# Performance work log

Measured on AMD Instinct MI355X. Metric: run time of the kernel, lower is better.

Reference implementation:

```python
import jax, jax.numpy as jnp
import numpy as np

N_NODES = 50000
N_EDGES = 800000
IN_CH = 128
OUT_CH = 64
HEADS = 4
NEG_SLOPE = 0.2  # PyG GATConv default


def setup_inputs() -> dict:
    key = jax.random.key(0)
    k1, k2, k3, k4, k5 = jax.random.split(key, 5)
    x = jax.random.normal(k1, (N_NODES, IN_CH), dtype=jnp.float32)
    edge_index = jax.random.randint(k2, (2, N_EDGES), 0, N_NODES, dtype=jnp.int64)
    W = jax.random.normal(k3, (HEADS * OUT_CH, IN_CH), dtype=jnp.float32) * (1.0 / np.sqrt(IN_CH))
    att_src = jax.random.normal(k4, (HEADS, OUT_CH), dtype=jnp.float32) * (1.0 / np.sqrt(OUT_CH))
    att_dst = jax.random.normal(k5, (HEADS, OUT_CH), dtype=jnp.float32) * (1.0 / np.sqrt(OUT_CH))
    bias = jnp.zeros((OUT_CH,), dtype=jnp.float32)
    return {"x": x, "edge_index": edge_index, "W": W,
            "att_src": att_src, "att_dst": att_dst, "bias": bias}


def reference(x, edge_index, W, att_src, att_dst, bias):
    # GAT2NO_NORM.forward in eval mode: dropout == identity.
    N = x.shape[0]
    H, C = att_src.shape
    # PyG GATConv adds self-loops by default.
    loop = jnp.arange(N, dtype=edge_index.dtype)
    src = jnp.concatenate([edge_index[0], loop])  # message source j
    dst = jnp.concatenate([edge_index[1], loop])  # message target i
    # Linear projection, reshape to heads: [N, H, C]
    h = (x @ W.T).reshape(N, H, C)
    # Per-node attention halves: [N, H]
    a_src = jnp.einsum('nhc,hc->nh', h, att_src)
    a_dst = jnp.einsum('nhc,hc->nh', h, att_dst)
    # Per-edge raw score, LeakyReLU: [E, H]
    e = jax.nn.leaky_relu(a_src[src] + a_dst[dst], NEG_SLOPE)
    # Segment (edge-)softmax over incoming edges of each dst node.
    m = jax.lax.stop_gradient(jax.ops.segment_max(e, dst, num_segments=N))
    ex = jnp.exp(e - m[dst])
    denom = jax.ops.segment_sum(ex, dst, num_segments=N)
    alpha = ex / denom[dst]  # self-loops guarantee denom > 0
    # Weighted scatter-sum of messages: [N, H, C]
    msg = h[src] * alpha[:, :, None]
    out = jax.ops.segment_sum(msg, dst, num_segments=N)
    # concat=False -> mean over heads, then bias, then ReLU (module wrapper)
    out = out.mean(axis=1) + bias
    return jax.nn.relu(out)
```

## Files before the change

### kernel.cpp

```cpp
#include <hip/hip_runtime.h>
#include <hip/hip_fp16.h>
#include <math.h>

#define N_NODES 50000
#define N_EDGES 800000
#define IN_CH 128
#define PROJ_CH 256
#define OUT_CH 64
#define HEADS 4
#define NEG_SLOPE 0.2f
#define CAP 80
#define PROJ_BLOCKS 782
#define GRID_BLOCKS 3125

typedef _Float16 f16x8 __attribute__((ext_vector_type(8)));
typedef _Float16 f16x4 __attribute__((ext_vector_type(4)));
typedef float    f32x4 __attribute__((ext_vector_type(4)));

__device__ __forceinline__ float leaky(float v) {
    return v > 0.f ? v : NEG_SLOPE * v;
}

__global__ __launch_bounds__(256) void prep_kernel(
    const float* __restrict__ W, _Float16* __restrict__ Wfrag, int* __restrict__ cnt)
{
    int t = blockIdx.x * 256 + threadIdx.x;
    if (t < N_NODES) cnt[t] = 0;
    if (t < 4096) {
        int lane = t & 63;
        int n0i  = (t >> 6) & 3;
        int w    = (t >> 8) & 3;
        int k0i  = t >> 10;
        int oc = w * 64 + n0i * 16 + (lane & 15);
        int kb = k0i * 32 + (lane >> 4) * 8;
        const float* src = W + (size_t)oc * IN_CH + kb;
        f16x8 v;
#pragma unroll
        for (int j = 0; j < 8; ++j) v[j] = (_Float16)src[j];
        *(f16x8*)(Wfrag + (size_t)t * 8) = v;
    }
}

__global__ __launch_bounds__(256) void mega_kernel(
    const float* __restrict__ x, const _Float16* __restrict__ Wfrag,
    const float* __restrict__ att_src, const float* __restrict__ att_dst,
    const int* __restrict__ ei, int* __restrict__ cnt, unsigned short* __restrict__ csr,
    _Float16* __restrict__ h, float* __restrict__ a_src, float* __restrict__ a_dst)
{
    __shared__ _Float16 xs[64 * 136];
    const int tid = threadIdx.x;
    const int bid = blockIdx.x;

    const int e = bid * 256 + tid;
    const int esrc = ei[e];
    const int edst = ei[N_EDGES + e];

    if (bid >= PROJ_BLOCKS) {
        int pos = atomicAdd(&cnt[edst], 1);
        if (pos < CAP) csr[edst * CAP + pos] = (unsigned short)esrc;
        return;
    }

    const int w    = tid >> 6;
    const int lane = tid & 63;
    const int q    = lane >> 4;
    const int l15  = lane & 15;
    const int nb   = bid * 64;

    f16x8 B[4][4];
#pragma unroll
    for (int k0i = 0; k0i < 4; ++k0i)
#pragma unroll
        for (int n0i = 0; n0i < 4; ++n0i)
            B[k0i][n0i] = *(const f16x8*)(Wfrag +
                (size_t)(((k0i * 4 + w) * 4 + n0i) * 64 + lane) * 8);

#pragma unroll
    for (int r = 0; r < 8; ++r) {
        int v   = r * 256 + tid;
        int row = v >> 5;
        int c4  = v & 31;
        int grow = nb + row;
        if (grow > N_NODES - 1) grow = N_NODES - 1;
        float4 xv = *(const float4*)(x + (size_t)grow * IN_CH + c4 * 4);
        f16x4 hv;
        hv[0] = (_Float16)xv.x; hv[1] = (_Float16)xv.y;
        hv[2] = (_Float16)xv.z; hv[3] = (_Float16)xv.w;
        *(f16x4*)&xs[row * 136 + c4 * 4] = hv;
    }
    __syncthreads();

    const int pos = atomicAdd(&cnt[edst], 1);

    f32x4 acc[4][4];
#pragma unroll
    for (int m0i = 0; m0i < 4; ++m0i)
#pragma unroll
        for (int n0i = 0; n0i < 4; ++n0i)
            acc[m0i][n0i] = (f32x4){0.f, 0.f, 0.f, 0.f};

#pragma unroll
    for (int k0i = 0; k0i < 4; ++k0i) {
        f16x8 A[4];
#pragma unroll
        for (int m0i = 0; m0i < 4; ++m0i)
            A[m0i] = *(const f16x8*)&xs[(m0i * 16 + l15) * 136 + k0i * 32 + q * 8];
#pragma unroll
        for (int n0i = 0; n0i < 4; ++n0i)
#pragma unroll
            for (int m0i = 0; m0i < 4; ++m0i)
                acc[m0i][n0i] = __builtin_amdgcn_mfma_f32_16x16x32_f16(
                    A[m0i], B[k0i][n0i], acc[m0i][n0i], 0, 0, 0);
    }

    float att_s[4], att_d[4];
#pragma unroll
    for (int n0i = 0; n0i < 4; ++n0i) {
        att_s[n0i] = att_src[w * 64 + n0i * 16 + l15];
        att_d[n0i] = att_dst[w * 64 + n0i * 16 + l15];
    }

#pragma unroll
    for (int m0i = 0; m0i < 4; ++m0i) {
        float vs[4], vd[4];
#pragma unroll
        for (int r = 0; r < 4; ++r) {
            float s = 0.f, d = 0.f;
#pragma unroll
            for (int n0i = 0; n0i < 4; ++n0i) {
                s = fmaf(acc[m0i][n0i][r], att_s[n0i], s);
                d = fmaf(acc[m0i][n0i][r], att_d[n0i], d);
            }
            vs[r] = s; vd[r] = d;
        }
#pragma unroll
        for (int off = 1; off < 16; off <<= 1) {
#pragma unroll
            for (int r = 0; r < 4; ++r) {
                vs[r] += __shfl_xor(vs[r], off, 64);
                vd[r] += __shfl_xor(vd[r], off, 64);
            }
        }
#pragma unroll
        for (int r = 0; r < 4; ++r) {
            int node = nb + m0i * 16 + q * 4 + r;
            if (l15 == 0 && node < N_NODES) {
                a_src[node * HEADS + w] = vs[r];
                a_dst[node * HEADS + w] = vd[r];
            }
        }
#pragma unroll
        for (int r = 0; r < 4; ++r) {
            int node = nb + m0i * 16 + q * 4 + r;
            if (node < N_NODES) {
#pragma unroll
                for (int n0i = 0; n0i < 4; ++n0i)
                    h[(size_t)node * PROJ_CH + w * 64 + n0i * 16 + l15] =
                        (_Float16)acc[m0i][n0i][r];
            }
        }
    }

    if (pos < CAP) csr[edst * CAP + pos] = (unsigned short)esrc;
}

__global__ __launch_bounds__(256) void aggregate_kernel(
    const _Float16* __restrict__ h, const float* __restrict__ a_src,
    const float* __restrict__ a_dst, const int* __restrict__ cnt,
    const unsigned short* __restrict__ csr, const float* __restrict__ bias,
    float* __restrict__ out)
{
    const int tid  = threadIdx.x;
    const int wave = tid >> 6;
    const int l    = tid & 63;
    const int i    = blockIdx.x * 4 + wave;

    __shared__ float lw_all[4][(CAP + 1) * 4];
    __shared__ int   lj_all[4][CAP + 1 + 3];
    float* lw = lw_all[wave];
    int*   lj = lj_all[wave];

    const int n    = min(cnt[i], CAP);
    const int base = i * CAP;
    const int h4   = l & 3;
    const float adh = a_dst[i * 4 + h4];

    float lsum = 0.f;
    {
        float ws = __expf(leaky(a_src[i * 4 + h4] + adh));
        if (l < 4) { lw[l] = ws; lsum = ws; }
        if (l == 0) lj[0] = i;
    }

    const int erel = l >> 2;
    for (int p0 = 0; p0 < n; p0 += 16) {
        int e = p0 + erel;
        bool valid = e < n;
        int j = valid ? (int)csr[base + e] : 0;
        float w = 0.f;
        if (valid) w = __expf(leaky(a_src[j * 4 + h4] + adh));
        lsum += w;
        lw[(e + 1) * 4 + h4] = w;
        if (h4 == 0) lj[e + 1] = j;
    }
#pragma unroll
    for (int off = 4; off < 64; off <<= 1) lsum += __shfl_xor(lsum, off, 64);

    __syncthreads();

    const int half_ = l >> 5;
    const int jj    = l & 31;
    const int hd    = jj >> 3;
    const int m_total = n + 1;
    const uint4* hv = (const uint4*)h;

    float acc[8];
#pragma unroll
    for (int k = 0; k < 8; ++k) acc[k] = 0.f;

    for (int qq = 0; qq < m_total; qq += 4) {
        int e0 = qq + half_;
        int e1 = e0 + 2;
        int i0 = (e0 < m_total) ? e0 : 0;
        int i1 = (e1 < m_total) ? e1 : 0;
        float w0 = (e0 < m_total) ? lw[i0 * 4 + hd] : 0.f;
        float w1 = (e1 < m_total) ? lw[i1 * 4 + hd] : 0.f;
        int j0 = lj[i0];
        int j1 = lj[i1];
        uint4 d0 = hv[(size_t)j0 * 32 + jj];
        uint4 d1 = hv[(size_t)j1 * 32 + jj];
        float2 a0 = __half22float2(*(const __half2*)&d0.x);
        float2 a1 = __half22float2(*(const __half2*)&d0.y);
        float2 a2 = __half22float2(*(const __half2*)&d0.z);
        float2 a3 = __half22float2(*(const __half2*)&d0.w);
        acc[0] = fmaf(w0, a0.x, acc[0]);
        acc[1] = fmaf(w0, a0.y, acc[1]);
        acc[2] = fmaf(w0, a1.x, acc[2]);
        acc[3] = fmaf(w0, a1.y, acc[3]);
        acc[4] = fmaf(w0, a2.x, acc[4]);
        acc[5] = fmaf(w0, a2.y, acc[5]);
        acc[6] = fmaf(w0, a3.x, acc[6]);
        acc[7] = fmaf(w0, a3.y, acc[7]);
        float2 b0 = __half22float2(*(const __half2*)&d1.x);
        float2 b1 = __half22float2(*(const __half2*)&d1.y);
        float2 b2 = __half22float2(*(const __half2*)&d1.z);
        float2 b3 = __half22float2(*(const __half2*)&d1.w);
        acc[0] = fmaf(w1, b0.x, acc[0]);
        acc[1] = fmaf(w1, b0.y, acc[1]);
        acc[2] = fmaf(w1, b1.x, acc[2]);
        acc[3] = fmaf(w1, b1.y, acc[3]);
        acc[4] = fmaf(w1, b2.x, acc[4]);
        acc[5] = fmaf(w1, b2.y, acc[5]);
        acc[6] = fmaf(w1, b3.x, acc[6]);
        acc[7] = fmaf(w1, b3.y, acc[7]);
    }

#pragma unroll
    for (int k = 0; k < 8; ++k) acc[k] += __shfl_xor(acc[k], 32, 64);

    float linv = 1.f / __shfl(lsum, hd, 64);
#pragma unroll
    for (int k = 0; k < 8; ++k) {
        float r = acc[k] * linv;
        r += __shfl_xor(r, 8, 64);
        r += __shfl_xor(r, 16, 64);
        acc[k] = r;
    }

    if (l < 8) {
        float* op = out + (size_t)i * OUT_CH + l * 8;
        float4 o0, o1;
        o0.x = fmaxf(0.25f * acc[0] + bias[l * 8 + 0], 0.f);
        o0.y = fmaxf(0.25f * acc[1] + bias[l * 8 + 1], 0.f);
        o0.z = fmaxf(0.25f * acc[2] + bias[l * 8 + 2], 0.f);
        o0.w = fmaxf(0.25f * acc[3] + bias[l * 8 + 3], 0.f);
        o1.x = fmaxf(0.25f * acc[4] + bias[l * 8 + 4], 0.f);
        o1.y = fmaxf(0.25f * acc[5] + bias[l * 8 + 5], 0.f);
        o1.z = fmaxf(0.25f * acc[6] + bias[l * 8 + 6], 0.f);
        o1.w = fmaxf(0.25f * acc[7] + bias[l * 8 + 7], 0.f);
        *(float4*)op = o0;
        *((float4*)op + 1) = o1;
    }
}

extern "C" void kernel_launch(void* const* d_in, const int* in_sizes, int n_in,
                              void* d_out, int out_size, void* d_ws, size_t ws_size,
                              hipStream_t stream)
{
    const float* x       = (const float*)d_in[0];
    const int*   ei      = (const int*)d_in[1];
    const float* W       = (const float*)d_in[2];
    const float* att_src = (const float*)d_in[3];
    const float* att_dst = (const float*)d_in[4];
    const float* bias    = (const float*)d_in[5];
    float* out = (float*)d_out;

    _Float16* h     = (_Float16*)d_ws;
    _Float16* Wfrag = h + (size_t)N_NODES * PROJ_CH;
    float* asrc  = (float*)(Wfrag + 4096 * 8);
    float* adst  = asrc + (size_t)N_NODES * HEADS;
    int*   cnt   = (int*)(adst + (size_t)N_NODES * HEADS);
    unsigned short* csr = (unsigned short*)(cnt + N_NODES);

    hipLaunchKernelGGL(prep_kernel, dim3(196), dim3(256), 0, stream,
                       W, Wfrag, cnt);
    hipLaunchKernelGGL(mega_kernel, dim3(GRID_BLOCKS), dim3(256), 0, stream,
                       x, Wfrag, att_src, att_dst, ei, cnt, csr, h, asrc, adst);
    hipLaunchKernelGGL(aggregate_kernel, dim3(N_NODES / 4), dim3(256), 0, stream,
                       h, asrc, adst, cnt, csr, bias, out);
}
```

Before: 206.4 us.

## Drop prep kernel, convert W in-kernel, use packed fp16 dot2 in aggregation

Removes the separate W-fragment prep kernel: each projection block now loads W in fp32 and converts it to fp16 MFMA fragments itself, and the counter reset becomes a memset. The aggregation loop now processes four edges per half-wave per iteration, packing pairs of fp16 features with perm and accumulating with fdot2 against fp16-packed weights, which exposes more loads in flight and uses fewer ALU ops. This trades a kernel launch for redundant W reads per block. The attention weights are rounded to fp16 (round toward zero), which loses some accuracy.

```diff
diff --git a/kernel.cpp b/kernel.cpp
--- a/kernel.cpp
+++ b/kernel.cpp
@@ -15,34 +15,19 @@
 
 typedef _Float16 f16x8 __attribute__((ext_vector_type(8)));
 typedef _Float16 f16x4 __attribute__((ext_vector_type(4)));
+typedef __fp16   hf2   __attribute__((ext_vector_type(2)));
 typedef float    f32x4 __attribute__((ext_vector_type(4)));
 
 __device__ __forceinline__ float leaky(float v) {
     return v > 0.f ? v : NEG_SLOPE * v;
 }
 
-__global__ __launch_bounds__(256) void prep_kernel(
-    const float* __restrict__ W, _Float16* __restrict__ Wfrag, int* __restrict__ cnt)
-{
-    int t = blockIdx.x * 256 + threadIdx.x;
-    if (t < N_NODES) cnt[t] = 0;
-    if (t < 4096) {
-        int lane = t & 63;
-        int n0i  = (t >> 6) & 3;
-        int w    = (t >> 8) & 3;
-        int k0i  = t >> 10;
-        int oc = w * 64 + n0i * 16 + (lane & 15);
-        int kb = k0i * 32 + (lane >> 4) * 8;
-        const float* src = W + (size_t)oc * IN_CH + kb;
-        f16x8 v;
-#pragma unroll
-        for (int j = 0; j < 8; ++j) v[j] = (_Float16)src[j];
-        *(f16x8*)(Wfrag + (size_t)t * 8) = v;
-    }
+__device__ __forceinline__ hf2 u32_as_h2(unsigned int u) {
+    union { unsigned int u; hf2 h; } c; c.u = u; return c.h;
 }
 
 __global__ __launch_bounds__(256) void mega_kernel(
-    const float* __restrict__ x, const _Float16* __restrict__ Wfrag,
+    const float* __restrict__ x, const float* __restrict__ W,
     const float* __restrict__ att_src, const float* __restrict__ att_dst,
     const int* __restrict__ ei, int* __restrict__ cnt, unsigned short* __restrict__ csr,
     _Float16* __restrict__ h, float* __restrict__ a_src, float* __restrict__ a_dst)
@@ -71,9 +56,18 @@
 #pragma unroll
     for (int k0i = 0; k0i < 4; ++k0i)
 #pragma unroll
-        for (int n0i = 0; n0i < 4; ++n0i)
-            B[k0i][n0i] = *(const f16x8*)(Wfrag +
-                (size_t)(((k0i * 4 + w) * 4 + n0i) * 64 + lane) * 8);
+        for (int n0i = 0; n0i < 4; ++n0i) {
+            const int oc = w * 64 + n0i * 16 + l15;
+            const float* src = W + (size_t)oc * IN_CH + k0i * 32 + q * 8;
+            float4 s0 = *(const float4*)src;
+            float4 s1 = *(const float4*)(src + 4);
+            f16x8 v;
+            v[0] = (_Float16)s0.x; v[1] = (_Float16)s0.y;
+            v[2] = (_Float16)s0.z; v[3] = (_Float16)s0.w;
+            v[4] = (_Float16)s1.x; v[5] = (_Float16)s1.y;
+            v[6] = (_Float16)s1.z; v[7] = (_Float16)s1.w;
+            B[k0i][n0i] = v;
+        }
 
 #pragma unroll
     for (int r = 0; r < 8; ++r) {
@@ -176,7 +170,7 @@
     const int i    = blockIdx.x * 4 + wave;
 
     __shared__ float lw_all[4][(CAP + 1) * 4];
-    __shared__ int   lj_all[4][CAP + 1 + 3];
+    __shared__ int   lj_all[4][CAP + 4];
     float* lw = lw_all[wave];
     int*   lj = lj_all[wave];
 
@@ -218,41 +212,37 @@
 #pragma unroll
     for (int k = 0; k < 8; ++k) acc[k] = 0.f;
 
-    for (int qq = 0; qq < m_total; qq += 4) {
-        int e0 = qq + half_;
-        int e1 = e0 + 2;
-        int i0 = (e0 < m_total) ? e0 : 0;
-        int i1 = (e1 < m_total) ? e1 : 0;
-        float w0 = (e0 < m_total) ? lw[i0 * 4 + hd] : 0.f;
-        float w1 = (e1 < m_total) ? lw[i1 * 4 + hd] : 0.f;
-        int j0 = lj[i0];
-        int j1 = lj[i1];
-        uint4 d0 = hv[(size_t)j0 * 32 + jj];
-        uint4 d1 = hv[(size_t)j1 * 32 + jj];
-        float2 a0 = __half22float2(*(const __half2*)&d0.x);
-        float2 a1 = __half22float2(*(const __half2*)&d0.y);
-        float2 a2 = __half22float2(*(const __half2*)&d0.z);
-        float2 a3 = __half22float2(*(const __half2*)&d0.w);
-        acc[0] = fmaf(w0, a0.x, acc[0]);
-        acc[1] = fmaf(w0, a0.y, acc[1]);
-        acc[2] = fmaf(w0, a1.x, acc[2]);
-        acc[3] = fmaf(w0, a1.y, acc[3]);
-        acc[4] = fmaf(w0, a2.x, acc[4]);
-        acc[5] = fmaf(w0, a2.y, acc[5]);
-        acc[6] = fmaf(w0, a3.x, acc[6]);
-        acc[7] = fmaf(w0, a3.y, acc[7]);
-        float2 b0 = __half22float2(*(const __half2*)&d1.x);
-        float2 b1 = __half22float2(*(const __half2*)&d1.y);
-        float2 b2 = __half22float2(*(const __half2*)&d1.z);
-        float2 b3 = __half22float2(*(const __half2*)&d1.w);
-        acc[0] = fmaf(w1, b0.x, acc[0]);
-        acc[1] = fmaf(w1, b0.y, acc[1]);
-        acc[2] = fmaf(w1, b1.x, acc[2]);
-        acc[3] = fmaf(w1, b1.y, acc[3]);
-        acc[4] = fmaf(w1, b2.x, acc[4]);
-        acc[5] = fmaf(w1, b2.y, acc[5]);
-        acc[6] = fmaf(w1, b3.x, acc[6]);
-        acc[7] = fmaf(w1, b3.y, acc[7]);
+    for (int qq = 0; qq < m_total; qq += 8) {
+        const int eb = qq + 4 * half_;
+        int ia[4]; float wa[4];
+#pragma unroll
+        for (int k = 0; k < 4; ++k) {
+            int e = eb + k;
+            ia[k] = (e < m_total) ? e : 0;
+            wa[k] = (e < m_total) ? lw[ia[k] * 4 + hd] : 0.f;
+        }
+        uint4 d0 = hv[(size_t)lj[ia[0]] * 32 + jj];
+        uint4 d1 = hv[(size_t)lj[ia[1]] * 32 + jj];
+        uint4 d2 = hv[(size_t)lj[ia[2]] * 32 + jj];
+        uint4 d3 = hv[(size_t)lj[ia[3]] * 32 + jj];
+        hf2 wab = __builtin_amdgcn_cvt_pkrtz(wa[0], wa[1]);
+        hf2 wcd = __builtin_amdgcn_cvt_pkrtz(wa[2], wa[3]);
+
+        const unsigned int* A0 = (const unsigned int*)&d0;
+        const unsigned int* A1 = (const unsigned int*)&d1;
+        const unsigned int* A2 = (const unsigned int*)&d2;
+        const unsigned int* A3 = (const unsigned int*)&d3;
+#pragma unroll
+        for (int k = 0; k < 4; ++k) {
+            unsigned int lo01 = __builtin_amdgcn_perm(A1[k], A0[k], 0x05040100u);
+            unsigned int hi01 = __builtin_amdgcn_perm(A1[k], A0[k], 0x07060302u);
+            acc[2 * k]     = __builtin_amdgcn_fdot2(u32_as_h2(lo01), wab, acc[2 * k], false);
+            acc[2 * k + 1] = __builtin_amdgcn_fdot2(u32_as_h2(hi01), wab, acc[2 * k + 1], false);
+            unsigned int lo23 = __builtin_amdgcn_perm(A3[k], A2[k], 0x05040100u);
+            unsigned int hi23 = __builtin_amdgcn_perm(A3[k], A2[k], 0x07060302u);
+            acc[2 * k]     = __builtin_amdgcn_fdot2(u32_as_h2(lo23), wcd, acc[2 * k], false);
+            acc[2 * k + 1] = __builtin_amdgcn_fdot2(u32_as_h2(hi23), wcd, acc[2 * k + 1], false);
+        }
     }
 
 #pragma unroll
@@ -295,17 +285,15 @@
     const float* bias    = (const float*)d_in[5];
     float* out = (float*)d_out;
 
-    _Float16* h     = (_Float16*)d_ws;
-    _Float16* Wfrag = h + (size_t)N_NODES * PROJ_CH;
-    float* asrc  = (float*)(Wfrag + 4096 * 8);
+    _Float16* h   = (_Float16*)d_ws;
+    float* asrc  = (float*)(h + (size_t)N_NODES * PROJ_CH);
     float* adst  = asrc + (size_t)N_NODES * HEADS;
     int*   cnt   = (int*)(adst + (size_t)N_NODES * HEADS);
     unsigned short* csr = (unsigned short*)(cnt + N_NODES);
 
-    hipLaunchKernelGGL(prep_kernel, dim3(196), dim3(256), 0, stream,
-                       W, Wfrag, cnt);
+    (void)hipMemsetAsync(cnt, 0, N_NODES * sizeof(int), stream);
     hipLaunchKernelGGL(mega_kernel, dim3(GRID_BLOCKS), dim3(256), 0, stream,
-                       x, Wfrag, att_src, att_dst, ei, cnt, csr, h, asrc, adst);
+                       x, W, att_src, att_dst, ei, cnt, csr, h, asrc, adst);
     hipLaunchKernelGGL(aggregate_kernel, dim3(N_NODES / 4), dim3(256), 0, stream,
                        h, asrc, adst, cnt, csr, bias, out);
 }
```

After: 196.0 us. 5.0% less time.
